# Optimization experiments

Measured on AMD Instinct MI355X. Metric: run time of the kernel, lower is better.

The kernel has to match this reference:

```python
import jax, jax.numpy as jnp
import numpy as np

B, L, D, DI, DS, DC, DTR = 128, 31, 1024, 2048, 16, 5, 64

def setup_inputs() -> dict:
    key = jax.random.key(0)
    ks = jax.random.split(key, 12)
    rn = lambda k, shp, s=0.02: jax.random.normal(k, shp, dtype=jnp.float32) * s
    return {
        "x": jax.random.normal(ks[0], (B, L, D), dtype=jnp.float32),
        "norm1_w": jnp.ones((D,), jnp.float32), "norm1_b": jnp.zeros((D,), jnp.float32),
        "in_proj_W": rn(ks[1], (2 * DI, D)),
        "conv_w": rn(ks[2], (DI, DC), 0.2), "conv_b": jnp.zeros((DI,), jnp.float32),
        "x_proj_W": rn(ks[3], (DTR + 2 * DS, DI)),
        "dt_proj_W": rn(ks[4], (DI, DTR), 0.1),
        "dt_proj_b": jnp.full((DI,), -4.6, dtype=jnp.float32),  # softplus^-1(~0.01)
        "A_log": jnp.tile(jnp.log(jnp.arange(1, DS + 1, dtype=jnp.float32))[None, :], (DI, 1)),
        "D_ssm": jnp.ones((DI,), jnp.float32),
        "out_proj_W": rn(ks[5], (D, DI)),
        "norm2_w": jnp.ones((D,), jnp.float32), "norm2_b": jnp.zeros((D,), jnp.float32),
        "ffn_W1": rn(ks[6], (2 * D, D)), "ffn_b1": jnp.zeros((2 * D,), jnp.float32),
        "ffn_W2": rn(ks[7], (D, 2 * D)), "ffn_b2": jnp.zeros((D,), jnp.float32),
        "cls_W1": rn(ks[8], (D, L * D)), "cls_b1": jnp.zeros((D,), jnp.float32),
        "cls_W2": rn(ks[9], (1, D)), "cls_b2": jnp.zeros((1,), jnp.float32),
    }

def _ln(x, w, b):
    m = x.mean(-1, keepdims=True)
    v = x.var(-1, keepdims=True)
    return (x - m) * jax.lax.rsqrt(v + 1e-5) * w + b

def _mamba(x, in_proj_W, conv_w, conv_b, x_proj_W, dt_proj_W, dt_proj_b, A_log, D_ssm, out_proj_W):
    # in_proj -> (u, z)
    xz = jnp.einsum('bld,ed->ble', x, in_proj_W)            # (B,L,2*DI)
    u, z = jnp.split(xz, 2, axis=-1)
    # causal depthwise conv1d (kernel DC) + SiLU
    xp = jnp.pad(u, ((0, 0), (DC - 1, 0), (0, 0)))
    uc = conv_b + sum(xp[:, k:k + L, :] * conv_w[:, k] for k in range(DC))
    uc = jax.nn.silu(uc)
    # input-dependent dt, B, C
    x_dbl = jnp.einsum('bld,ed->ble', uc, x_proj_W)         # (B,L,DTR+2*DS)
    dt, Bm, Cm = jnp.split(x_dbl, [DTR, DTR + DS], axis=-1)
    dt = jax.nn.softplus(jnp.einsum('blr,dr->bld', dt, dt_proj_W) + dt_proj_b)
    A = -jnp.exp(A_log)                                      # (DI,DS)
    def step(h, ins):
        dt_t, B_t, C_t, u_t = ins                            # (B,DI),(B,DS),(B,DS),(B,DI)
        dA = jnp.exp(dt_t[:, :, None] * A)                   # (B,DI,DS)
        h = h * dA + dt_t[:, :, None] * B_t[:, None, :] * u_t[:, :, None]
        y = jnp.einsum('bds,bs->bd', h, C_t)
        return h, y
    h0 = jnp.zeros((u.shape[0], DI, DS), u.dtype)
    _, ys = jax.lax.scan(step, h0, (dt.transpose(1, 0, 2), Bm.transpose(1, 0, 2),
                                    Cm.transpose(1, 0, 2), uc.transpose(1, 0, 2)))
    y = ys.transpose(1, 0, 2) + uc * D_ssm                   # skip term D*u
    y = y * jax.nn.silu(z)                                   # gate
    return jnp.einsum('bld,ed->ble', y, out_proj_W)

def reference(x, norm1_w, norm1_b, in_proj_W, conv_w, conv_b, x_proj_W, dt_proj_W,
              dt_proj_b, A_log, D_ssm, out_proj_W, norm2_w, norm2_b, ffn_W1, ffn_b1,
              ffn_W2, ffn_b2, cls_W1, cls_b1, cls_W2, cls_b2):
    # single encoder block (n_layers=1), dropout = identity (eval)
    res = x
    h = _ln(x, norm1_w, norm1_b)
    h = _mamba(h, in_proj_W, conv_w, conv_b, x_proj_W, dt_proj_W, dt_proj_b,
               A_log, D_ssm, out_proj_W)
    x = res + h
    res = x
    h = _ln(x, norm2_w, norm2_b)
    h = jax.nn.silu(jnp.einsum('bld,ed->ble', h, ffn_W1) + ffn_b1)
    h = jnp.einsum('ble,de->bld', h, ffn_W2) + ffn_b2
    x = res + h
    # classifier: Flatten -> Linear -> SiLU -> Linear
    flat = x.reshape(x.shape[0], -1)                          # (B, L*D)
    c = jax.nn.silu(flat @ cls_W1.T + cls_b1)
    out = c @ cls_W2.T + cls_b2                               # (B,1)
    return (out, x)
```

## Files before the change

kernel.cpp:

```cpp
#include <hip/hip_runtime.h>
#include <cstddef>
#include <cstdint>

#define B_   128
#define L_   31
#define D_   1024
#define DI_  2048
#define DS_  16
#define DC_  5
#define DTR_ 64
#define ROWS (B_ * L_)
#define KCLS (L_ * D_)

#define W_IN  0
#define W_OUT 4194304
#define W_F1  6291456
#define W_F2  8388608
#define W_XP  10485760
#define W_DT  10747904
#define WTOT  10878976

typedef unsigned short u16;
typedef __attribute__((ext_vector_type(8))) short s16x8;
typedef __attribute__((ext_vector_type(4))) float f32x4;

__device__ __forceinline__ float silu_f(float x) { return x / (1.0f + __expf(-x)); }

__device__ __forceinline__ u16 f2b(float f) {
    union { float f; uint32_t u; } c; c.f = f;
    uint32_t u = c.u + 0x7FFF + ((c.u >> 16) & 1);
    return (u16)(u >> 16);
}
__device__ __forceinline__ float b2f(u16 b) {
    union { uint32_t u; float f; } c; c.u = ((uint32_t)b) << 16;
    return c.f;
}
__device__ __forceinline__ uint32_t pack2(float lo, float hi) {
    return (uint32_t)f2b(lo) | ((uint32_t)f2b(hi) << 16);
}
__device__ __forceinline__ void cvt8(const float* __restrict__ s, u16* __restrict__ d) {
    const float4* p = (const float4*)s;
    float4 a = p[0], b = p[1];
    uint4 r;
    r.x = pack2(a.x, a.y); r.y = pack2(a.z, a.w);
    r.z = pack2(b.x, b.y); r.w = pack2(b.z, b.w);
    *(uint4*)d = r;
}

#define GLD16(g, s) __builtin_amdgcn_global_load_lds( \
    (const __attribute__((address_space(1))) void*)(g), \
    (__attribute__((address_space(3))) void*)(s), 16, 0, 0)

__global__ __launch_bounds__(256) void f2b_all_kernel(
    const float* __restrict__ inW, const float* __restrict__ outW,
    const float* __restrict__ f1W, const float* __restrict__ f2W,
    const float* __restrict__ xpW, const float* __restrict__ dtW,
    u16* __restrict__ wbuf)
{
    int g = blockIdx.x * 256 + threadIdx.x;
    if (g < 524288) { cvt8(inW + (size_t)g * 8, wbuf + W_IN + (size_t)g * 8); return; }
    g -= 524288;
    if (g < 262144) { cvt8(outW + (size_t)g * 8, wbuf + W_OUT + (size_t)g * 8); return; }
    g -= 262144;
    if (g < 262144) { cvt8(f1W + (size_t)g * 8, wbuf + W_F1 + (size_t)g * 8); return; }
    g -= 262144;
    if (g < 262144) { cvt8(f2W + (size_t)g * 8, wbuf + W_F2 + (size_t)g * 8); return; }
    g -= 262144;
    if (g < 32768) {
        const int row = g >> 8, col8 = (g & 255) * 8;
        u16* d = wbuf + W_XP + (size_t)row * 2048 + col8;
        if (row < 96) cvt8(xpW + (size_t)row * 2048 + col8, d);
        else *(uint4*)d = make_uint4(0, 0, 0, 0);
        return;
    }
    g -= 32768;
    if (g < 16384) cvt8(dtW + (size_t)g * 8, wbuf + W_DT + (size_t)g * 8);
}

__global__ __launch_bounds__(256) void ln_kernel(const float* __restrict__ x,
                                                 const float* __restrict__ w,
                                                 const float* __restrict__ b,
                                                 u16* __restrict__ y)
{
    const int row = blockIdx.x;
    const float* xr = x + (size_t)row * D_;
    float v[4];
    float sum = 0.f, sq = 0.f;
#pragma unroll
    for (int i = 0; i < 4; i++) {
        v[i] = xr[threadIdx.x + i * 256];
        sum += v[i];
        sq  += v[i] * v[i];
    }
#pragma unroll
    for (int o = 32; o > 0; o >>= 1) {
        sum += __shfl_down(sum, o, 64);
        sq  += __shfl_down(sq, o, 64);
    }
    __shared__ float red[8];
    const int wid = threadIdx.x >> 6;
    if ((threadIdx.x & 63) == 0) { red[wid] = sum; red[4 + wid] = sq; }
    __syncthreads();
    sum = red[0] + red[1] + red[2] + red[3];
    sq  = red[4] + red[5] + red[6] + red[7];
    const float mean = sum * (1.0f / D_);
    const float var  = sq * (1.0f / D_) - mean * mean;
    const float rstd = rsqrtf(var + 1e-5f);
    u16* yr = y + (size_t)row * D_;
#pragma unroll
    for (int i = 0; i < 4; i++) {
        const int c = threadIdx.x + i * 256;
        yr[c] = f2b((v[i] - mean) * rstd * w[c] + b[c]);
    }
}

__global__ __launch_bounds__(256) void ln2_fuse_kernel(const float* __restrict__ x,
                                                       const u16* __restrict__ p0,
                                                       const u16* __restrict__ p1,
                                                       const float* __restrict__ w,
                                                       const float* __restrict__ b,
                                                       float* __restrict__ x2,
                                                       u16* __restrict__ y)
{
    const int row = blockIdx.x;
    const size_t base = (size_t)row * D_;
    const int c4 = threadIdx.x * 4;
    float4 xv = *(const float4*)(x + base + c4);
    uint2 p0v = *(const uint2*)(p0 + base + c4);
    uint2 p1v = *(const uint2*)(p1 + base + c4);
    float v[4];
    v[0] = xv.x + b2f((u16)p0v.x)         + b2f((u16)p1v.x);
    v[1] = xv.y + b2f((u16)(p0v.x >> 16)) + b2f((u16)(p1v.x >> 16));
    v[2] = xv.z + b2f((u16)p0v.y)         + b2f((u16)(p1v.y));
    v[3] = xv.w + b2f((u16)(p0v.y >> 16)) + b2f((u16)(p1v.y >> 16));
    *(float4*)(x2 + base + c4) = make_float4(v[0], v[1], v[2], v[3]);
    float sum = v[0] + v[1] + v[2] + v[3];
    float sq  = v[0]*v[0] + v[1]*v[1] + v[2]*v[2] + v[3]*v[3];
#pragma unroll
    for (int o = 32; o > 0; o >>= 1) {
        sum += __shfl_down(sum, o, 64);
        sq  += __shfl_down(sq, o, 64);
    }
    __shared__ float red[8];
    const int wid = threadIdx.x >> 6;
    if ((threadIdx.x & 63) == 0) { red[wid] = sum; red[4 + wid] = sq; }
    __syncthreads();
    sum = red[0] + red[1] + red[2] + red[3];
    sq  = red[4] + red[5] + red[6] + red[7];
    const float mean = sum * (1.0f / D_);
    const float var  = sq * (1.0f / D_) - mean * mean;
    const float rstd = rsqrtf(var + 1e-5f);
    float4 wv = *(const float4*)(w + c4);
    float4 bv = *(const float4*)(b + c4);
    uint2 r;
    r.x = pack2((v[0] - mean) * rstd * wv.x + bv.x, (v[1] - mean) * rstd * wv.y + bv.y);
    r.y = pack2((v[2] - mean) * rstd * wv.z + bv.z, (v[3] - mean) * rstd * wv.w + bv.w);
    *(uint2*)(y + base + c4) = r;
}

__global__ __launch_bounds__(256) void add3_bias_kernel(const float* __restrict__ x2,
                                                        const u16* __restrict__ q0,
                                                        const u16* __restrict__ q1,
                                                        const float* __restrict__ b2,
                                                        float* __restrict__ x3)
{
    const int i = blockIdx.x * 256 + threadIdx.x;
    float4 a  = ((const float4*)x2)[i];
    uint2 c0 = ((const uint2*)q0)[i];
    uint2 c1 = ((const uint2*)q1)[i];
    float4 bb = ((const float4*)b2)[i & 255];
    float4 r;
    r.x = a.x + b2f((u16)c0.x)         + b2f((u16)c1.x)         + bb.x;
    r.y = a.y + b2f((u16)(c0.x >> 16)) + b2f((u16)(c1.x >> 16)) + bb.y;
    r.z = a.z + b2f((u16)c0.y)         + b2f((u16)c1.y)         + bb.z;
    r.w = a.w + b2f((u16)(c0.y >> 16)) + b2f((u16)(c1.y >> 16)) + bb.w;
    ((float4*)x3)[i] = r;
}

template <int ACT, bool BIAS, int OUT>
__global__ __launch_bounds__(256) void gemm128_bk64(
    const u16* __restrict__ A, const u16* __restrict__ W,
    const float* __restrict__ bias, void* __restrict__ Cout,
    int M, int K, int Nout, int kLen)
{
    __shared__ __align__(16) u16 As[128 * 64];
    __shared__ __align__(16) u16 Bs[128 * 64];
    const int tid = threadIdx.x;
    const int l = tid & 63, w = tid >> 6;
    const int bm = blockIdx.y * 128, bn = blockIdx.x * 128;
    const int kOff = blockIdx.z * kLen;

    const int srow = tid >> 3;
    const int sg   = tid & 7;
    const int sgx  = sg ^ (srow & 7);
    const u16* gA = A + (size_t)(bm + srow) * K + kOff + sgx * 8;
    const u16* gB = W + (size_t)(bn + srow) * K + kOff + sgx * 8;
    const int soff = srow * 64 + sg * 8;

    const int lane15 = l & 15, lhi = l >> 4;
    const int key = lane15 & 7;
    const int wr = w >> 1, wc = w & 1;
    const u16* fArow = As + (wr * 64 + lane15) * 64;
    const u16* fBrow = Bs + (wc * 64 + lane15) * 64;

    f32x4 acc[4][4] = {};

    for (int kk = 0; kk < kLen; kk += 64) {
#pragma unroll
        for (int c = 0; c < 4; c++) {
            GLD16(gA + (size_t)c * 32 * K, As + c * 2048 + soff);
            GLD16(gB + (size_t)c * 32 * K, Bs + c * 2048 + soff);
        }
        gA += 64; gB += 64;
        __syncthreads();
#pragma unroll
        for (int ks = 0; ks < 2; ks++) {
            const int gsel = ((ks * 4 + lhi) ^ key) * 8;
            s16x8 af[4], bfr[4];
#pragma unroll
            for (int mi = 0; mi < 4; mi++) af[mi]  = *(const s16x8*)(fArow + mi * 16 * 64 + gsel);
#pragma unroll
            for (int ni = 0; ni < 4; ni++) bfr[ni] = *(const s16x8*)(fBrow + ni * 16 * 64 + gsel);
#pragma unroll
            for (int mi = 0; mi < 4; mi++)
#pragma unroll
                for (int ni = 0; ni < 4; ni++)
                    acc[mi][ni] = __builtin_amdgcn_mfma_f32_16x16x32_bf16(
                        af[mi], bfr[ni], acc[mi][ni], 0, 0, 0);
        }
        __syncthreads();
    }

#pragma unroll
    for (int ni = 0; ni < 4; ni++) {
        const int col = bn + wc * 64 + ni * 16 + lane15;
        if (col >= Nout) continue;
        const float bv = BIAS ? bias[col] : 0.0f;
#pragma unroll
        for (int mi = 0; mi < 4; mi++) {
#pragma unroll
            for (int r = 0; r < 4; r++) {
                const int row = bm + wr * 64 + mi * 16 + lhi * 4 + r;
                float v = acc[mi][ni][r] + bv;
                if (ACT == 1) v = silu_f(v);
                if (ACT == 2) v = (v > 20.0f) ? v : log1pf(__expf(v));
                if (OUT == 1) ((u16*)Cout)[(size_t)row * Nout + col] = f2b(v);
                if (OUT == 2) atomicAdd(&((float*)Cout)[(size_t)row * Nout + col], v);
                if (OUT == 3) ((float*)Cout)[((size_t)blockIdx.z * M + row) * Nout + col] = v;
                if (OUT == 4) ((u16*)Cout)[((size_t)blockIdx.z * M + row) * Nout + col] = f2b(v);
            }
        }
    }
}

#define KCH 512
__global__ __launch_bounds__(256) void gemm_cls_mfma(
    const float* __restrict__ A, const float* __restrict__ W,
    float* __restrict__ C)
{
    __shared__ __align__(16) u16 As[128 * 32];
    __shared__ __align__(16) u16 Bs[128 * 32];
    const int tid = threadIdx.x;
    const int l = tid & 63, w = tid >> 6;
    const int bn = blockIdx.x * 128;
    const int k0 = blockIdx.y * KCH;

    const int sr  = l >> 2;
    const int sgl = l & 3;
    const int row = w * 16 + sr;
    const int skw = ((sgl ^ (sr & 3))) * 8;
    const float* gA0 = A + (size_t)row * KCLS + k0 + sgl * 8;
    const float* gA1 = gA0 + (size_t)64 * KCLS;
    const float* gB0 = W + (size_t)(bn + row) * KCLS + k0 + sgl * 8;
    const float* gB1 = gB0 + (size_t)64 * KCLS;
    u16* lA0 = As + row * 32 + skw;  u16* lA1 = lA0 + 64 * 32;
    u16* lB0 = Bs + row * 32 + skw;  u16* lB1 = lB0 + 64 * 32;

    const int lane15 = l & 15, lhi = l >> 4;
    const int wr = w >> 1, wc = w & 1;
    const int rsel = (lhi ^ (lane15 & 3)) * 8;
    const u16* fA = As + (wr * 64 + lane15) * 32 + rsel;
    const u16* fB = Bs + (wc * 64 + lane15) * 32 + rsel;

    f32x4 acc[4][4] = {};

    float4 a00 = *(const float4*)(gA0);  float4 a01 = *(const float4*)(gA0 + 4);
    float4 a10 = *(const float4*)(gA1);  float4 a11 = *(const float4*)(gA1 + 4);
    float4 b00 = *(const float4*)(gB0);  float4 b01 = *(const float4*)(gB0 + 4);
    float4 b10 = *(const float4*)(gB1);  float4 b11 = *(const float4*)(gB1 + 4);

    for (int ks = 0; ks < KCH / 32; ks++) {
        if (ks) {
            asm volatile("" ::: "memory");
            __builtin_amdgcn_s_barrier();
            asm volatile("" ::: "memory");
        }
        uint4 r;
        r.x = pack2(a00.x, a00.y); r.y = pack2(a00.z, a00.w);
        r.z = pack2(a01.x, a01.y); r.w = pack2(a01.z, a01.w);
        *(uint4*)lA0 = r;
        r.x = pack2(a10.x, a10.y); r.y = pack2(a10.z, a10.w);
        r.z = pack2(a11.x, a11.y); r.w = pack2(a11.z, a11.w);
        *(uint4*)lA1 = r;
        r.x = pack2(b00.x, b00.y); r.y = pack2(b00.z, b00.w);
        r.z = pack2(b01.x, b01.y); r.w = pack2(b01.z, b01.w);
        *(uint4*)lB0 = r;
        r.x = pack2(b10.x, b10.y); r.y = pack2(b10.z, b10.w);
        r.z = pack2(b11.x, b11.y); r.w = pack2(b11.z, b11.w);
        *(uint4*)lB1 = r;
        if (ks + 1 < KCH / 32) {
            gA0 += 32; gA1 += 32; gB0 += 32; gB1 += 32;
            a00 = *(const float4*)(gA0);  a01 = *(const float4*)(gA0 + 4);
            a10 = *(const float4*)(gA1);  a11 = *(const float4*)(gA1 + 4);
            b00 = *(const float4*)(gB0);  b01 = *(const float4*)(gB0 + 4);
            b10 = *(const float4*)(gB1);  b11 = *(const float4*)(gB1 + 4);
        }
        asm volatile("s_waitcnt lgkmcnt(0)" ::: "memory");
        __builtin_amdgcn_s_barrier();
        asm volatile("" ::: "memory");
        s16x8 af[4], bfr[4];
#pragma unroll
        for (int mi = 0; mi < 4; mi++) af[mi]  = *(const s16x8*)(fA + mi * 16 * 32);
#pragma unroll
        for (int ni = 0; ni < 4; ni++) bfr[ni] = *(const s16x8*)(fB + ni * 16 * 32);
#pragma unroll
        for (int mi = 0; mi < 4; mi++)
#pragma unroll
            for (int ni = 0; ni < 4; ni++)
                acc[mi][ni] = __builtin_amdgcn_mfma_f32_16x16x32_bf16(
                    af[mi], bfr[ni], acc[mi][ni], 0, 0, 0);
    }

#pragma unroll
    for (int ni = 0; ni < 4; ni++) {
        const int col = bn + wc * 64 + ni * 16 + lane15;
#pragma unroll
        for (int mi = 0; mi < 4; mi++) {
#pragma unroll
            for (int r = 0; r < 4; r++) {
                const int m = wr * 64 + mi * 16 + lhi * 4 + r;
                atomicAdd(&C[(size_t)m * 1024 + col], acc[mi][ni][r]);
            }
        }
    }
}

__global__ __launch_bounds__(128) void conv_silu_kernel(const u16* __restrict__ xz,
                                                        const float* __restrict__ cw,
                                                        const float* __restrict__ cb,
                                                        u16* __restrict__ uc)
{
    const int b  = blockIdx.y;
    const int d0 = (blockIdx.x * 128 + threadIdx.x) * 8;
    const u16* up = xz + (size_t)b * L_ * (2 * DI_) + d0;
    u16* op = uc + (size_t)b * L_ * DI_ + d0;

    float wreg[8][DC_];
    float bias[8];
#pragma unroll
    for (int j = 0; j < 8; j++) {
        bias[j] = cb[d0 + j];
#pragma unroll
        for (int k = 0; k < DC_; k++) wreg[j][k] = cw[(d0 + j) * DC_ + k];
    }

    uint4 win[DC_];
#pragma unroll
    for (int k = 0; k < DC_; k++) win[k] = make_uint4(0, 0, 0, 0);

    for (int l = 0; l < L_; l++) {
#pragma unroll
        for (int k = 0; k < DC_ - 1; k++) win[k] = win[k + 1];
        win[DC_ - 1] = *(const uint4*)(up + (size_t)l * (2 * DI_));
        float acc[8];
#pragma unroll
        for (int j = 0; j < 8; j++) acc[j] = bias[j];
#pragma unroll
        for (int k = 0; k < DC_; k++) {
            const uint32_t uw[4] = {win[k].x, win[k].y, win[k].z, win[k].w};
#pragma unroll
            for (int j = 0; j < 8; j++)
                acc[j] = fmaf(b2f((u16)(uw[j >> 1] >> ((j & 1) * 16))), wreg[j][k], acc[j]);
        }
        uint4 r;
        r.x = pack2(silu_f(acc[0]), silu_f(acc[1]));
        r.y = pack2(silu_f(acc[2]), silu_f(acc[3]));
        r.z = pack2(silu_f(acc[4]), silu_f(acc[5]));
        r.w = pack2(silu_f(acc[6]), silu_f(acc[7]));
        *(uint4*)(op + (size_t)l * DI_) = r;
    }
}

__global__ __launch_bounds__(256) void dtext_kernel(const float* __restrict__ xdbl,
                                                    u16* __restrict__ dtb)
{
    const int idx = blockIdx.x * 256 + threadIdx.x;
    const int row = idx >> 4, c4 = (idx & 15) * 4;
    float4 v = *(const float4*)(xdbl + (size_t)row * 96 + c4);
    uint2 r;
    r.x = pack2(v.x, v.y); r.y = pack2(v.z, v.w);
    *(uint2*)(dtb + (size_t)row * 64 + c4) = r;
}

__global__ __launch_bounds__(256) void scan_kernel(const u16* __restrict__ dt,
                                                   const u16* __restrict__ uc,
                                                   const u16* __restrict__ xz,
                                                   const float* __restrict__ xdbl,
                                                   const float* __restrict__ A_log,
                                                   const float* __restrict__ D_ssm,
                                                   u16* __restrict__ y)
{
    const int idx = blockIdx.x * 256 + threadIdx.x;
    const int d = idx & (DI_ - 1);
    const int b = idx >> 11;
    float A[DS_];
#pragma unroll
    for (int s = 0; s < DS_; s++) A[s] = -__expf(A_log[d * DS_ + s]);
    const float Dv = D_ssm[d];
    float h[DS_] = {};
    for (int l = 0; l < L_; l++) {
        const size_t bl = (size_t)b * L_ + l;
        const float dtv = b2f(dt[bl * DI_ + d]);
        const float uv  = b2f(uc[bl * DI_ + d]);
        const float zv  = b2f(xz[bl * (2 * DI_) + DI_ + d]);
        const float* Bp = xdbl + bl * (DTR_ + 2 * DS_) + DTR_;
        const float* Cp = Bp + DS_;
        float yv = 0.f;
#pragma unroll
        for (int s = 0; s < DS_; s++) {
            h[s] = fmaf(h[s], __expf(dtv * A[s]), dtv * Bp[s] * uv);
            yv = fmaf(h[s], Cp[s], yv);
        }
        yv = fmaf(uv, Dv, yv);
        yv *= silu_f(zv);
        y[bl * DI_ + d] = f2b(yv);
    }
}

__global__ __launch_bounds__(256) void cls2_kernel(const float* __restrict__ c,
                                                   const float* __restrict__ b1,
                                                   const float* __restrict__ W2,
                                                   const float* __restrict__ b2,
                                                   float* __restrict__ out)
{
    const int b = blockIdx.x;
    float s = 0.f;
    for (int n = threadIdx.x; n < D_; n += 256) {
        float v = c[b * D_ + n] + b1[n];
        v = silu_f(v);
        s = fmaf(v, W2[n], s);
    }
#pragma unroll
    for (int o = 32; o > 0; o >>= 1) s += __shfl_down(s, o, 64);
    __shared__ float red[4];
    const int wid = threadIdx.x >> 6;
    if ((threadIdx.x & 63) == 0) red[wid] = s;
    __syncthreads();
    if (threadIdx.x == 0) out[b] = red[0] + red[1] + red[2] + red[3] + b2[0];
}

extern "C" void kernel_launch(void* const* d_in, const int* in_sizes, int n_in,
                              void* d_out, int out_size, void* d_ws, size_t ws_size,
                              hipStream_t stream)
{
    const float* x         = (const float*)d_in[0];
    const float* n1w       = (const float*)d_in[1];
    const float* n1b       = (const float*)d_in[2];
    const float* in_projW  = (const float*)d_in[3];
    const float* conv_w    = (const float*)d_in[4];
    const float* conv_b    = (const float*)d_in[5];
    const float* x_projW   = (const float*)d_in[6];
    const float* dt_projW  = (const float*)d_in[7];
    const float* dt_projb  = (const float*)d_in[8];
    const float* A_log     = (const float*)d_in[9];
    const float* D_ssm     = (const float*)d_in[10];
    const float* out_projW = (const float*)d_in[11];
    const float* n2w       = (const float*)d_in[12];
    const float* n2b       = (const float*)d_in[13];
    const float* ffn_W1    = (const float*)d_in[14];
    const float* ffn_b1    = (const float*)d_in[15];
    const float* ffn_W2    = (const float*)d_in[16];
    const float* ffn_b2    = (const float*)d_in[17];
    const float* cls_W1    = (const float*)d_in[18];
    const float* cls_b1    = (const float*)d_in[19];
    const float* cls_W2    = (const float*)d_in[20];
    const float* cls_b2    = (const float*)d_in[21];

    u16* base   = (u16*)d_ws;
    u16* xz_b   = base;
    u16* uc_b   = xz_b + (size_t)ROWS * 4096;
    u16* dt_b   = uc_b + (size_t)ROWS * 2048;
    u16* y_b    = dt_b + (size_t)ROWS * 2048;
    u16* h_b    = y_b + (size_t)ROWS * 2048;
    float* x2   = (float*)(h_b + (size_t)ROWS * 1024);
    float* xdbl = x2 + (size_t)ROWS * 1024;
    u16* dtb    = (u16*)(xdbl + (size_t)ROWS * 96);
    u16* wbuf   = dtb + (size_t)ROWS * 64;
    float* clsh = (float*)(wbuf + (size_t)WTOT);
    u16* pq     = (u16*)(clsh + (size_t)B_ * D_);

    float* outv = (float*)d_out;
    float* x3   = outv + B_;

    f2b_all_kernel<<<dim3(5312), dim3(256), 0, stream>>>(
        in_projW, out_projW, ffn_W1, ffn_W2, x_projW, dt_projW, wbuf);
    ln_kernel<<<dim3(ROWS), dim3(256), 0, stream>>>(x, n1w, n1b, h_b);
    gemm128_bk64<0, false, 1><<<dim3(32, 31, 1), dim3(256), 0, stream>>>(
        h_b, wbuf + W_IN, nullptr, xz_b, ROWS, D_, 2 * DI_, D_);
    conv_silu_kernel<<<dim3(2, B_), dim3(128), 0, stream>>>(xz_b, conv_w, conv_b, uc_b);
    hipMemsetAsync(xdbl, 0, (size_t)ROWS * 96 * sizeof(float), stream);
    gemm128_bk64<0, false, 2><<<dim3(1, 31, 16), dim3(256), 0, stream>>>(
        uc_b, wbuf + W_XP, nullptr, xdbl, ROWS, DI_, DTR_ + 2 * DS_, 128);
    dtext_kernel<<<dim3(ROWS * 16 / 256), dim3(256), 0, stream>>>(xdbl, dtb);
    gemm128_bk64<2, true, 1><<<dim3(16, 31, 1), dim3(256), 0, stream>>>(
        dtb, wbuf + W_DT, dt_projb, dt_b, ROWS, DTR_, DI_, DTR_);
    scan_kernel<<<dim3(B_ * DI_ / 256), dim3(256), 0, stream>>>(
        dt_b, uc_b, xz_b, xdbl, A_log, D_ssm, y_b);
    gemm128_bk64<0, false, 4><<<dim3(8, 31, 2), dim3(256), 0, stream>>>(
        y_b, wbuf + W_OUT, nullptr, pq, ROWS, DI_, D_, 1024);
    ln2_fuse_kernel<<<dim3(ROWS), dim3(256), 0, stream>>>(
        x, pq, pq + (size_t)ROWS * D_, n2w, n2b, x2, h_b);
    gemm128_bk64<1, true, 1><<<dim3(16, 31, 1), dim3(256), 0, stream>>>(
        h_b, wbuf + W_F1, ffn_b1, uc_b, ROWS, D_, 2 * D_, D_);
    gemm128_bk64<0, false, 4><<<dim3(8, 31, 2), dim3(256), 0, stream>>>(
        uc_b, wbuf + W_F2, nullptr, pq, ROWS, 2 * D_, D_, 1024);
    add3_bias_kernel<<<dim3(ROWS * D_ / 4 / 256), dim3(256), 0, stream>>>(
        x2, pq, pq + (size_t)ROWS * D_, ffn_b2, x3);
    hipMemsetAsync(clsh, 0, (size_t)B_ * D_ * sizeof(float), stream);
    gemm_cls_mfma<<<dim3(1024 / 128, KCLS / KCH), dim3(256), 0, stream>>>(x3, cls_W1, clsh);
    cls2_kernel<<<dim3(B_), dim3(256), 0, stream>>>(clsh, cls_b1, cls_W2, cls_b2, outv);
}
```

Baseline: 384.7 us.

## Fuse dt_proj matvec and softplus into the selective scan kernel

Removes the dtext bf16 conversion kernel and the dt_proj GEMM, and drops the dt_proj weight conversion. Each scan thread now holds its 64-wide dt_proj row in registers and computes dt = softplus(xdbl_dt·w + b) in fp32 per timestep. This saves two launches and the round trip of a ROWS×2048 bf16 dt tensor through global memory. In exchange the scan does 64 extra FMAs per step and carries 64 extra registers, which may lower occupancy. The xdbl row loads are broadcast across a block since every thread with the same batch index reads the same row.

New measurement: 394.1 us. 2.5% more time.

```diff
diff --git a/kernel.cpp b/kernel.cpp
--- a/kernel.cpp
+++ b/kernel.cpp
@@ -17,8 +17,7 @@
 #define W_F1  6291456
 #define W_F2  8388608
 #define W_XP  10485760
-#define W_DT  10747904
-#define WTOT  10878976
+#define WTOT  10747904
 
 typedef unsigned short u16;
 typedef __attribute__((ext_vector_type(8))) short s16x8;
@@ -54,8 +53,7 @@
 __global__ __launch_bounds__(256) void f2b_all_kernel(
     const float* __restrict__ inW, const float* __restrict__ outW,
     const float* __restrict__ f1W, const float* __restrict__ f2W,
-    const float* __restrict__ xpW, const float* __restrict__ dtW,
-    u16* __restrict__ wbuf)
+    const float* __restrict__ xpW, u16* __restrict__ wbuf)
 {
     int g = blockIdx.x * 256 + threadIdx.x;
     if (g < 524288) { cvt8(inW + (size_t)g * 8, wbuf + W_IN + (size_t)g * 8); return; }
@@ -71,10 +69,7 @@
         u16* d = wbuf + W_XP + (size_t)row * 2048 + col8;
         if (row < 96) cvt8(xpW + (size_t)row * 2048 + col8, d);
         else *(uint4*)d = make_uint4(0, 0, 0, 0);
-        return;
-    }
-    g -= 32768;
-    if (g < 16384) cvt8(dtW + (size_t)g * 8, wbuf + W_DT + (size_t)g * 8);
+    }
 }
 
 __global__ __launch_bounds__(256) void ln_kernel(const float* __restrict__ x,
@@ -391,21 +386,11 @@
     }
 }
 
-__global__ __launch_bounds__(256) void dtext_kernel(const float* __restrict__ xdbl,
-                                                    u16* __restrict__ dtb)
-{
-    const int idx = blockIdx.x * 256 + threadIdx.x;
-    const int row = idx >> 4, c4 = (idx & 15) * 4;
-    float4 v = *(const float4*)(xdbl + (size_t)row * 96 + c4);
-    uint2 r;
-    r.x = pack2(v.x, v.y); r.y = pack2(v.z, v.w);
-    *(uint2*)(dtb + (size_t)row * 64 + c4) = r;
-}
-
-__global__ __launch_bounds__(256) void scan_kernel(const u16* __restrict__ dt,
+__global__ __launch_bounds__(256) void scan_kernel(const float* __restrict__ xdbl,
+                                                   const float* __restrict__ Wdt,
+                                                   const float* __restrict__ db,
                                                    const u16* __restrict__ uc,
                                                    const u16* __restrict__ xz,
-                                                   const float* __restrict__ xdbl,
                                                    const float* __restrict__ A_log,
                                                    const float* __restrict__ D_ssm,
                                                    u16* __restrict__ y)
@@ -417,13 +402,31 @@
 #pragma unroll
     for (int s = 0; s < DS_; s++) A[s] = -__expf(A_log[d * DS_ + s]);
     const float Dv = D_ssm[d];
+    const float dbv = db[d];
+    float wdt[DTR_];
+#pragma unroll
+    for (int r4 = 0; r4 < DTR_ / 4; r4++) {
+        float4 wv = *(const float4*)(Wdt + (size_t)d * DTR_ + r4 * 4);
+        wdt[r4 * 4 + 0] = wv.x; wdt[r4 * 4 + 1] = wv.y;
+        wdt[r4 * 4 + 2] = wv.z; wdt[r4 * 4 + 3] = wv.w;
+    }
     float h[DS_] = {};
     for (int l = 0; l < L_; l++) {
         const size_t bl = (size_t)b * L_ + l;
-        const float dtv = b2f(dt[bl * DI_ + d]);
+        const float* xr = xdbl + bl * (DTR_ + 2 * DS_);
+        float dtacc = dbv;
+#pragma unroll
+        for (int r4 = 0; r4 < DTR_ / 4; r4++) {
+            float4 xv = *(const float4*)(xr + r4 * 4);
+            dtacc = fmaf(xv.x, wdt[r4 * 4 + 0], dtacc);
+            dtacc = fmaf(xv.y, wdt[r4 * 4 + 1], dtacc);
+            dtacc = fmaf(xv.z, wdt[r4 * 4 + 2], dtacc);
+            dtacc = fmaf(xv.w, wdt[r4 * 4 + 3], dtacc);
+        }
+        const float dtv = (dtacc > 20.0f) ? dtacc : log1pf(__expf(dtacc));
         const float uv  = b2f(uc[bl * DI_ + d]);
         const float zv  = b2f(xz[bl * (2 * DI_) + DI_ + d]);
-        const float* Bp = xdbl + bl * (DTR_ + 2 * DS_) + DTR_;
+        const float* Bp = xr + DTR_;
         const float* Cp = Bp + DS_;
         float yv = 0.f;
 #pragma unroll
@@ -489,21 +492,19 @@
     u16* base   = (u16*)d_ws;
     u16* xz_b   = base;
     u16* uc_b   = xz_b + (size_t)ROWS * 4096;
-    u16* dt_b   = uc_b + (size_t)ROWS * 2048;
-    u16* y_b    = dt_b + (size_t)ROWS * 2048;
+    u16* y_b    = uc_b + (size_t)ROWS * 2048;
     u16* h_b    = y_b + (size_t)ROWS * 2048;
     float* x2   = (float*)(h_b + (size_t)ROWS * 1024);
     float* xdbl = x2 + (size_t)ROWS * 1024;
-    u16* dtb    = (u16*)(xdbl + (size_t)ROWS * 96);
-    u16* wbuf   = dtb + (size_t)ROWS * 64;
+    u16* wbuf   = (u16*)(xdbl + (size_t)ROWS * 96);
     float* clsh = (float*)(wbuf + (size_t)WTOT);
     u16* pq     = (u16*)(clsh + (size_t)B_ * D_);
 
     float* outv = (float*)d_out;
     float* x3   = outv + B_;
 
-    f2b_all_kernel<<<dim3(5312), dim3(256), 0, stream>>>(
-        in_projW, out_projW, ffn_W1, ffn_W2, x_projW, dt_projW, wbuf);
+    f2b_all_kernel<<<dim3(5248), dim3(256), 0, stream>>>(
+        in_projW, out_projW, ffn_W1, ffn_W2, x_projW, wbuf);
     ln_kernel<<<dim3(ROWS), dim3(256), 0, stream>>>(x, n1w, n1b, h_b);
     gemm128_bk64<0, false, 1><<<dim3(32, 31, 1), dim3(256), 0, stream>>>(
         h_b, wbuf + W_IN, nullptr, xz_b, ROWS, D_, 2 * DI_, D_);
@@ -511,11 +512,8 @@
     hipMemsetAsync(xdbl, 0, (size_t)ROWS * 96 * sizeof(float), stream);
     gemm128_bk64<0, false, 2><<<dim3(1, 31, 16), dim3(256), 0, stream>>>(
         uc_b, wbuf + W_XP, nullptr, xdbl, ROWS, DI_, DTR_ + 2 * DS_, 128);
-    dtext_kernel<<<dim3(ROWS * 16 / 256), dim3(256), 0, stream>>>(xdbl, dtb);
-    gemm128_bk64<2, true, 1><<<dim3(16, 31, 1), dim3(256), 0, stream>>>(
-        dtb, wbuf + W_DT, dt_projb, dt_b, ROWS, DTR_, DI_, DTR_);
     scan_kernel<<<dim3(B_ * DI_ / 256), dim3(256), 0, stream>>>(
-        dt_b, uc_b, xz_b, xdbl, A_log, D_ssm, y_b);
+        xdbl, dt_projW, dt_projb, uc_b, xz_b, A_log, D_ssm, y_b);
     gemm128_bk64<0, false, 4><<<dim3(8, 31, 2), dim3(256), 0, stream>>>(
         y_b, wbuf + W_OUT, nullptr, pq, ROWS, DI_, D_, 1024);
     ln2_fuse_kernel<<<dim3(ROWS), dim3(256), 0, stream>>>(
```
